# Kernel tuning notes

Hardware: AMD Instinct MI355X
Metric: run time of the kernel (lower is better)

The kernel has to match this reference:

```python
import jax, jax.numpy as jnp
import numpy as np

NUM_V = 20000
N_EDGES = 160000
IN_CH, OUT_CH = 16, 32
IN_ORDER = OUT_ORDER = MID_ORDER = 2
N_RINGS = 2
BAND_LIMIT = 2
NUM_SAMPLES = 7


def build_kernel_basis(n_in, n_out, bl):
    """Equivariant kernel basis [num_bases, 2*bl+1, 2*n_out+1, 2*n_in+1].
    Freq axis layout: [const, cos(t), sin(t), cos(2t), sin(2t), ...] matching precomp."""
    Din, Dout, F = 2 * n_in + 1, 2 * n_out + 1, 2 * bl + 1
    I = np.eye(2)
    E = np.array([[0., -1.], [1., 0.]])   # rotation by pi/2
    S = np.array([[1., 0.], [0., -1.]])   # reflection
    ES = E @ S
    sl = lambda m: slice(0, 1) if m == 0 else slice(2 * m - 1, 2 * m + 1)
    bases = []

    def add(f, cos_blk, sin_blk, m, n):
        if f > bl:
            return
        B = np.zeros((F, Dout, Din))
        if f == 0:
            B[0, sl(m), sl(n)] = cos_blk
        else:
            B[2 * f - 1, sl(m), sl(n)] = cos_blk
            B[2 * f, sl(m), sl(n)] = sin_blk
        bases.append(B)

    for m in range(n_out + 1):
        for n in range(n_in + 1):
            if m == 0 and n == 0:
                add(0, np.ones((1, 1)), None, 0, 0)
            elif n == 0:  # scalar -> order-m pair: R(m t) e1, R(m t) e2
                add(m, np.array([[1.], [0.]]), np.array([[0.], [1.]]), m, 0)
                add(m, np.array([[0.], [1.]]), np.array([[-1.], [0.]]), m, 0)
            elif m == 0:  # order-n pair -> scalar: rows of R(-n t)
                add(n, np.array([[1., 0.]]), np.array([[0., 1.]]), 0, n)
                add(n, np.array([[0., 1.]]), np.array([[-1., 0.]]), 0, n)
            else:
                d = m - n
                f = abs(d)
                sg = 1.0 if d >= 0 else -1.0
                add(f, I, sg * E, m, n)          # R(d t)
                add(f, E, -sg * I, m, n)         # R(d t + pi/2)
                add(m + n, S, ES, m, n)          # R((m+n) t) S
                add(m + n, ES, -S, m, n)         # R((m+n) t + pi/2) S
    return np.stack(bases).astype(np.float32)


def fourier_mats(order, n):
    th = 2 * np.pi * np.arange(n) / n
    cols = [np.ones(n)]
    for m in range(1, order + 1):
        cols += [np.cos(m * th), np.sin(m * th)]
    T = np.stack(cols, 1)                              # [n_samples, 2*order+1]
    scale = np.array([1.0] + [2.0] * (2 * order)) / n
    Tinv = (T * scale).T                               # [2*order+1, n_samples]
    return jnp.asarray(T, jnp.float32), jnp.asarray(Tinv, jnp.float32)


def rep_act(x, alpha, order):
    """Gauge transport: rotate order-m feature pairs by m*alpha. x: [E,C,2*order+1]."""
    parts = [x[:, :, :1]]
    for m in range(1, order + 1):
        c = jnp.cos(m * alpha)[:, None]
        s = jnp.sin(m * alpha)[:, None]
        a, b = x[:, :, 2 * m - 1], x[:, :, 2 * m]
        parts.append(jnp.stack([c * a - s * b, s * a + c * b], axis=-1))
    return jnp.concatenate(parts, axis=-1)


def gem_conv(x, edge_index, precomp, connection, K, W, b, in_order):
    src, dst = edge_index[1], edge_index[0]
    xt = rep_act(x[src], connection, in_order)               # [E, Cin, Din] gather + transport
    wk = jnp.einsum('bfij,broc->froicj', K, W)               # fold basis with ring weights (small)
    t = jnp.einsum('ecj,froicj->efroi', xt, wk)              # per-edge freq/ring responses
    msg = jnp.einsum('efr,efroi->eoi', precomp, t)           # [E, Cout, Dout]
    out = jax.ops.segment_sum(msg, dst, num_segments=NUM_V)  # scatter-add to vertices
    return out.at[:, :, 0].add(b)                            # bias on scalar component


def regular_relu(x, order):
    T, Tinv = fourier_mats(order, NUM_SAMPLES)
    s = jnp.einsum('vcd,sd->vcs', x, T)   # irrep -> regular samples
    return jnp.einsum('vcs,ds->vcd', jax.nn.relu(s), Tinv)


def setup_inputs() -> dict:
    key = jax.random.key(0)
    k = jax.random.split(key, 8)
    nb = build_kernel_basis(IN_ORDER, MID_ORDER, BAND_LIMIT).shape[0]  # 19
    Din = 2 * IN_ORDER + 1
    x = jax.random.normal(k[0], (NUM_V, IN_CH, Din), jnp.float32)
    edge_index = jax.random.randint(k[1], (2, N_EDGES), 0, NUM_V, dtype=jnp.int32)
    precomp = jax.random.normal(k[2], (N_EDGES, 2 * BAND_LIMIT + 1, N_RINGS), jnp.float32)
    connection = jax.random.uniform(k[3], (N_EDGES,), jnp.float32) * (2 * np.pi)
    W1 = jax.random.normal(k[4], (nb, N_RINGS, OUT_CH, IN_CH), jnp.float32) * 0.1
    W2 = jax.random.normal(k[5], (nb, N_RINGS, OUT_CH, OUT_CH), jnp.float32) * 0.05
    W_lin = jax.random.normal(k[6], (OUT_CH, IN_CH), jnp.float32) * 0.1
    zeros = lambda: jnp.zeros((OUT_CH,), jnp.float32)
    return {"x": x, "edge_index": edge_index, "precomp": precomp, "connection": connection,
            "W1": W1, "b1": zeros(), "W2": W2, "b2": zeros(), "W_lin": W_lin, "b_lin": zeros()}


def reference(x, edge_index, precomp, connection, W1, b1, W2, b2, W_lin, b_lin):
    K = jnp.asarray(build_kernel_basis(IN_ORDER, MID_ORDER, BAND_LIMIT))  # orders equal -> shared basis
    y = gem_conv(x, edge_index, precomp, connection, K, W1, b1, IN_ORDER)
    y = regular_relu(y, MID_ORDER)
    y = gem_conv(y, edge_index, precomp, connection, K, W2, b2, MID_ORDER)
    res = jnp.einsum('vcd,oc->vod', x, W_lin) + b_lin[None, :, None]  # 1x1 conv residual
    o = min(y.shape[2], res.shape[2])
    y = y.at[:, :, :o].add(res[:, :, :o])
    return regular_relu(y, OUT_ORDER)
```

## Files before the change

### kernel.cpp

```cpp
#include <hip/hip_runtime.h>
#include <hip/hip_bf16.h>
#include <cstdint>

#define NV     20000
#define NE     160000
#define IC1    16
#define OC     32
#define DIN    5
#define NSLOT  49
#define NOUT   160
struct SlotTables {
    int n;
    int b[64], f[64], i[64], j[64];
    float v[64];
};

constexpr SlotTables make_slots() {
    SlotTables T{};
    float K[19][5][5][5] = {};
    int nb = 0;
    const int BL = 2;
    auto add = [&](int f, const float (*cb)[2], const float (*sb)[2],
                   int m, int n) {
        if (f > BL) return;
        int r0 = (m == 0) ? 0 : (2 * m - 1), nr = (m == 0) ? 1 : 2;
        int c0 = (n == 0) ? 0 : (2 * n - 1), nc = (n == 0) ? 1 : 2;
        for (int a = 0; a < nr; a++)
            for (int bb = 0; bb < nc; bb++) {
                if (f == 0) {
                    K[nb][0][r0 + a][c0 + bb] = cb[a][bb];
                } else {
                    K[nb][2 * f - 1][r0 + a][c0 + bb] = cb[a][bb];
                    K[nb][2 * f    ][r0 + a][c0 + bb] = sb[a][bb];
                }
            }
        nb++;
    };
    const float ONE[2][2]  = {{1, 0}, {0, 0}};
    const float I2[2][2]   = {{1, 0}, {0, 1}};
    const float E2[2][2]   = {{0, -1}, {1, 0}};
    const float S2[2][2]   = {{1, 0}, {0, -1}};
    const float ES2[2][2]  = {{0, 1}, {1, 0}};
    const float NS2[2][2]  = {{-1, 0}, {0, 1}};
    const float C10[2][2]  = {{1, 0}, {0, 0}};
    const float C01[2][2]  = {{0, 0}, {1, 0}};
    const float CM10[2][2] = {{-1, 0}, {0, 0}};
    const float R10[2][2]  = {{1, 0}, {0, 0}};
    const float R01[2][2]  = {{0, 1}, {0, 0}};
    const float RM10[2][2] = {{-1, 0}, {0, 0}};

    for (int m = 0; m <= 2; m++)
        for (int n = 0; n <= 2; n++) {
            if (m == 0 && n == 0) {
                add(0, ONE, ONE, 0, 0);
            } else if (n == 0) {
                add(m, C10, C01, m, 0);
                add(m, C01, CM10, m, 0);
            } else if (m == 0) {
                add(n, R10, R01, 0, n);
                add(n, R01, RM10, 0, n);
            } else {
                int d = m - n;
                int f = d >= 0 ? d : -d;
                float sg = d >= 0 ? 1.f : -1.f;
                const float sgE[2][2]  = {{0, -sg}, {sg, 0}};
                const float msgI[2][2] = {{-sg, 0}, {0, -sg}};
                add(f, I2, sgE, m, n);
                add(f, E2, msgI, m, n);
                add(m + n, S2, ES2, m, n);
                add(m + n, ES2, NS2, m, n);
            }
        }
    T.n = 0;
    for (int i = 0; i < 5; i++)
        for (int b = 0; b < nb; b++)
            for (int f = 0; f < 5; f++)
                for (int j = 0; j < 5; j++)
                    if (K[b][f][i][j] != 0.0f) {
                        T.b[T.n] = b; T.f[T.n] = f; T.i[T.n] = i;
                        T.j[T.n] = j; T.v[T.n] = K[b][f][i][j];
                        T.n++;
                    }
    return T;
}

constexpr SlotTables SL = make_slots();
static_assert(SL.n == NSLOT, "expect 49 kernel-basis nonzeros");

__device__ __forceinline__ uint32_t bf16_rne(float f) {
    uint32_t u = __float_as_uint(f);
    u += 0x7fffu + ((u >> 16) & 1u);
    return u >> 16;
}

typedef __attribute__((ext_vector_type(8))) short bf16x8;
typedef __attribute__((ext_vector_type(4))) float f32x4;

template<int C>
__global__ __launch_bounds__(256) void build_M(const float* __restrict__ W,
                                               float* __restrict__ M) {
    int t = blockIdx.x * 256 + threadIdx.x;
    const int K = C * 50;
    if (t >= K * NOUT) return;
    int n = t % NOUT, k = t / NOUT;
    int o = n / 5, i = n % 5;
    int c = k / 50, r50 = k % 50;
    int j = r50 / 10, q = r50 % 10;
    int f = q >> 1, r = q & 1;
    float acc = 0.f;
    #pragma unroll
    for (int s = 0; s < NSLOT; s++) {
        if (SL.j[s] == j && SL.f[s] == f && SL.i[s] == i)
            acc += SL.v[s] * W[(size_t)((SL.b[s] * 2 + r) * 32 + o) * C + c];
    }
    M[(size_t)k * NOUT + n] = acc;
}

template<int K>
__global__ __launch_bounds__(256) void build_Mfrag(const float* __restrict__ M,
                                                   uint32_t* __restrict__ Mf) {
    int t = blockIdx.x * 256 + threadIdx.x;
    const int total = (K / 32) * 10 * 64 * 4;
    if (t >= total) return;
    int a = t & 3;
    int idx = t >> 2;
    int lane = idx & 63; idx >>= 6;
    int nt = idx % 10;
    int ck = idx / 10;
    int col = nt * 16 + (lane & 15);
    int k0 = ck * 32 + (lane >> 4) * 8 + 2 * a;
    uint32_t lo = bf16_rne(M[(size_t)k0 * NOUT + col]);
    uint32_t hi = bf16_rne(M[(size_t)(k0 + 1) * NOUT + col]);
    Mf[t] = lo | (hi << 16);
}

__global__ __launch_bounds__(256) void hist_k(const int* __restrict__ ei,
                                              int* __restrict__ counts) {
    int e = blockIdx.x * 256 + threadIdx.x;
    if (e < NE) atomicAdd(&counts[ei[e]], 1);
}

__global__ __launch_bounds__(1024) void scan_k(const int* __restrict__ counts,
                                               int* __restrict__ cursor) {
    __shared__ int part[1024];
    int t = threadIdx.x;
    int base = t * 20;
    int local[20];
    int s = 0;
    #pragma unroll
    for (int k = 0; k < 20; k++) {
        int idx = base + k;
        int c = (idx < NV) ? counts[idx] : 0;
        local[k] = c; s += c;
    }
    part[t] = s;
    __syncthreads();
    for (int off = 1; off < 1024; off <<= 1) {
        int add = (t >= off) ? part[t - off] : 0;
        __syncthreads();
        part[t] += add;
        __syncthreads();
    }
    int run = (t == 0) ? 0 : part[t - 1];
    #pragma unroll
    for (int k = 0; k < 20; k++) {
        int idx = base + k;
        if (idx < NV) { cursor[idx] = run; run += local[k]; }
    }
}

__global__ __launch_bounds__(256) void scatter_k(const int* __restrict__ ei,
                                                 int* __restrict__ cursor,
                                                 int* __restrict__ order) {
    int e = blockIdx.x * 256 + threadIdx.x;
    if (e >= NE) return;
    int pos = atomicAdd(&cursor[ei[e]], 1);
    order[pos] = e;
}

__global__ __launch_bounds__(256) void edge_pack(const int* __restrict__ ei,
                                                 const float* __restrict__ pre,
                                                 const float* __restrict__ conn,
                                                 const int* __restrict__ order,
                                                 int* __restrict__ SRC,
                                                 float4* __restrict__ REC) {
    int k = blockIdx.x * 256 + threadIdx.x;
    if (k > NE) return;
    if (k == NE) {
        SRC[NE] = 0;
        REC[(size_t)NE * 3 + 0] = float4{0.f, 0.f, 0.f, 0.f};
        REC[(size_t)NE * 3 + 1] = float4{0.f, 0.f, 0.f, 0.f};
        REC[(size_t)NE * 3 + 2] = float4{0.f, 0.f, 0.f, 0.f};
        return;
    }
    int e = order[k];
    SRC[k] = ei[NE + e];
    float al = conn[e];
    float c1 = __cosf(al), s1 = __sinf(al);
    const float* pp = pre + (size_t)e * 10;
    REC[(size_t)k * 3 + 0] = float4{c1, s1, pp[0], pp[1]};
    REC[(size_t)k * 3 + 1] = float4{pp[2], pp[3], pp[4], pp[5]};
    REC[(size_t)k * 3 + 2] = float4{pp[6], pp[7], pp[8], pp[9]};
}

template<int C>
__global__ __launch_bounds__(256) void zbuild4(const float* __restrict__ xin,
                                               const int*   __restrict__ SRC,
                                               const float4* __restrict__ REC,
                                               const int* __restrict__ cursor,
                                               uint32_t* __restrict__ Z,
                                               int v0, int v1) {
    __shared__ uint32_t st[3200];
    int tid = threadIdx.x;
    int t = blockIdx.x * 256 + tid;
    int pair = t >> 1, h = t & 1;
    int npairs = (v1 - v0) * C;
    bool valid = pair < npairs;
    int c = pair % C;
    int v = v0 + (valid ? pair / C : 0);
    int beg = 0, end = 0;
    if (valid) { beg = (v == 0) ? 0 : cursor[v - 1]; end = cursor[v]; }

    float acc[25];
    #pragma unroll
    for (int z = 0; z < 25; z++) acc[z] = 0.f;

    int k = beg;
    if (k < end) {
        int kn = (k + 1 < end) ? k + 1 : NE;
        int sC = SRC[k];
        int sN = SRC[kn];
        const float4* rp = REC + (size_t)k * 3;
        float4 r0 = rp[0], r1 = rp[1], r2 = rp[2];
        const float* xb = xin + ((size_t)sC * C + c) * DIN;
        float x0 = xb[0], x1 = xb[1], x2 = xb[2], x3 = xb[3], x4 = xb[4];
        while (true) {
            bool more = (k + 1 < end);
            int kn2 = (k + 2 < end) ? k + 2 : NE;
            int sN2 = SRC[kn2];
            const float* xbn = xin + ((size_t)sN * C + c) * DIN;
            float y0 = xbn[0], y1 = xbn[1], y2 = xbn[2], y3 = xbn[3],
                  y4 = xbn[4];
            const float4* rpn = REC + (size_t)kn * 3;
            float4 n0 = rpn[0], n1 = rpn[1], n2 = rpn[2];
            float c1 = r0.x, s1 = r0.y;
            float c2 = c1 * c1 - s1 * s1, s2 = 2.f * c1 * s1;
            float xt[5];
            xt[0] = x0;
            xt[1] = c1 * x1 - s1 * x2;
            xt[2] = s1 * x1 + c1 * x2;
            xt[3] = c2 * x3 - s2 * x4;
            xt[4] = s2 * x3 + c2 * x4;
            float ph[5];
            ph[0] = h ? r1.w : r0.z;
            ph[1] = h ? r2.x : r0.w;
            ph[2] = h ? r2.y : r1.x;
            ph[3] = h ? r2.z : r1.y;
            ph[4] = h ? r2.w : r1.z;
            #pragma unroll
            for (int j = 0; j < 5; j++)
                #pragma unroll
                for (int w = 0; w < 5; w++)
                    acc[j * 5 + w] = fmaf(xt[j], ph[w], acc[j * 5 + w]);
            if (!more) break;
            k += 1;
            r0 = n0; r1 = n1; r2 = n2;
            x0 = y0; x1 = y1; x2 = y2; x3 = y3; x4 = y4;
            sN = sN2; kn = kn2;
        }
    }
    uint32_t* sb = st + (tid >> 1) * 25;
    #pragma unroll
    for (int j = 0; j < 5; j++) {
        float q5v = __shfl_xor(acc[j * 5 + 0], 1);
        if (h == 0) {
            sb[j * 5 + 0] = bf16_rne(acc[j * 5 + 0]) | (bf16_rne(acc[j * 5 + 1]) << 16);
            sb[j * 5 + 1] = bf16_rne(acc[j * 5 + 2]) | (bf16_rne(acc[j * 5 + 3]) << 16);
            sb[j * 5 + 2] = bf16_rne(acc[j * 5 + 4]) | (bf16_rne(q5v) << 16);
        } else {
            sb[j * 5 + 3] = bf16_rne(acc[j * 5 + 1]) | (bf16_rne(acc[j * 5 + 2]) << 16);
            sb[j * 5 + 4] = bf16_rne(acc[j * 5 + 3]) | (bf16_rne(acc[j * 5 + 4]) << 16);
        }
    }
    __syncthreads();
    size_t gbase = (size_t)blockIdx.x * 3200;
    int pbase = blockIdx.x * 128;
    for (int i = tid; i < 3200; i += 256)
        if (pbase + i / 25 < npairs) Z[gbase + i] = st[i];
}

template<int K>
__global__ __launch_bounds__(256) void gemm_mfma(const uint32_t* __restrict__ Z,
                                                 const uint32_t* __restrict__ Mf,
                                                 float* __restrict__ Y,
                                                 int rows) {
    constexpr int NC = K / 32;
    __shared__ uint4 Bs[2][640];
    int t = threadIdx.x;
    int lane = t & 63;
    int wave = t >> 6;
    int r0 = blockIdx.x * 64 + wave * 16;
    int mrow = lane & 15;
    int q = lane >> 4;
    int ra = r0 + mrow;
    if (ra >= rows) ra = rows - 1;
    const uint32_t* za = Z + (size_t)ra * (K / 2) + q * 4;
    const uint4* mfg = (const uint4*)Mf + lane;

    auto stage = [&](int ck, int nb) {
        const uint4* gp = mfg + (size_t)ck * 640;
        for (int i = wave; i < 10; i += 4)
            __builtin_amdgcn_global_load_lds(
                (const __attribute__((address_space(1))) void*)(gp + i * 64),
                (__attribute__((address_space(3))) void*)(&Bs[nb][i * 64]),
                16, 0, 0);
    };

    f32x4 acc[10];
    #pragma unroll
    for (int nt = 0; nt < 10; nt++) acc[nt] = {0.f, 0.f, 0.f, 0.f};

    stage(0, 0);
    bf16x8 af = *(const bf16x8*)za;
    __syncthreads();

    for (int ck = 0; ck < NC; ck++) {
        int buf = ck & 1;
        bf16x8 af_n = af;
        if (ck + 1 < NC) {
            stage(ck + 1, buf ^ 1);
            af_n = *(const bf16x8*)(za + (ck + 1) * 16);
        }
        bf16x8 bf[10];
        #pragma unroll
        for (int nt = 0; nt < 10; nt++)
            bf[nt] = *(const bf16x8*)&Bs[buf][nt * 64 + lane];
        #pragma unroll
        for (int nt = 0; nt < 10; nt++)
            acc[nt] = __builtin_amdgcn_mfma_f32_16x16x32_bf16(af, bf[nt],
                                                              acc[nt], 0, 0, 0);
        af = af_n;
        __syncthreads();
    }
    #pragma unroll
    for (int reg = 0; reg < 4; reg++) {
        int rr = r0 + q * 4 + reg;
        if (rr < rows) {
            float* yb = Y + (size_t)rr * NOUT + (lane & 15);
            #pragma unroll
            for (int nt = 0; nt < 10; nt++) yb[nt * 16] = acc[nt][reg];
        }
    }
}

__device__ __forceinline__ void fourier_relu(float d0, float d1, float d2,
                                             float d3, float d4, float* out5) {
    float o0 = 0, o1 = 0, o2 = 0, o3 = 0, o4 = 0;
    #pragma unroll
    for (int k = 0; k < 7; k++) {
        float th = (float)k * (6.28318530717958647692f / 7.0f);
        float ck = __cosf(th), sk = __sinf(th);
        float c2k = ck * ck - sk * sk, s2k = 2.f * ck * sk;
        float sv = d0 + ck * d1 + sk * d2 + c2k * d3 + s2k * d4;
        sv = fmaxf(sv, 0.f);
        o0 += sv; o1 += sv * ck; o2 += sv * sk; o3 += sv * c2k; o4 += sv * s2k;
    }
    const float i7 = 1.0f / 7.0f;
    out5[0] = o0 * i7; out5[1] = o1 * (2.f * i7); out5[2] = o2 * (2.f * i7);
    out5[3] = o3 * (2.f * i7); out5[4] = o4 * (2.f * i7);
}

__global__ __launch_bounds__(256) void relu_mid(float* __restrict__ y,
                                                const float* __restrict__ b1) {
    int t = blockIdx.x * 256 + threadIdx.x;
    if (t >= NV * 32) return;
    int ch = t & 31;
    float* yb = y + (size_t)t * 5;
    float r[5];
    fourier_relu(yb[0] + b1[ch], yb[1], yb[2], yb[3], yb[4], r);
    #pragma unroll
    for (int d = 0; d < 5; d++) yb[d] = r[d];
}

__global__ __launch_bounds__(256) void final_k(const float* __restrict__ y2,
                                               const float* __restrict__ x,
                                               const float* __restrict__ Wl,
                                               const float* __restrict__ bl,
                                               const float* __restrict__ b2,
                                               float* __restrict__ out) {
    int t = blockIdx.x * 256 + threadIdx.x;
    if (t >= NV * 32) return;
    int o = t & 31;
    int v = t >> 5;
    float r0 = 0, r1 = 0, r2 = 0, r3 = 0, r4 = 0;
    const float* xb = x + (size_t)v * (IC1 * DIN);
    const float* wl = Wl + o * IC1;
    #pragma unroll
    for (int c = 0; c < IC1; c++) {
        float w = wl[c];
        r0 = fmaf(w, xb[c*5+0], r0); r1 = fmaf(w, xb[c*5+1], r1);
        r2 = fmaf(w, xb[c*5+2], r2); r3 = fmaf(w, xb[c*5+3], r3);
        r4 = fmaf(w, xb[c*5+4], r4);
    }
    float blo = bl[o];
    const float* yb = y2 + (size_t)t * 5;
    float d0 = yb[0] + b2[o] + r0 + blo;
    float d1 = yb[1] + r1 + blo;
    float d2 = yb[2] + r2 + blo;
    float d3 = yb[3] + r3 + blo;
    float d4 = yb[4] + r4 + blo;
    float r[5];
    fourier_relu(d0, d1, d2, d3, d4, r);
    float* ob = out + (size_t)t * 5;
    #pragma unroll
    for (int d = 0; d < 5; d++) ob[d] = r[d];
}

extern "C" void kernel_launch(void* const* d_in, const int* in_sizes, int n_in,
                              void* d_out, int out_size, void* d_ws, size_t ws_size,
                              hipStream_t stream) {
    const float* x    = (const float*)d_in[0];
    const int*   ei   = (const int*)  d_in[1];
    const float* pre  = (const float*)d_in[2];
    const float* conn = (const float*)d_in[3];
    const float* W1   = (const float*)d_in[4];
    const float* b1   = (const float*)d_in[5];
    const float* W2   = (const float*)d_in[6];
    const float* b2   = (const float*)d_in[7];
    const float* Wl   = (const float*)d_in[8];
    const float* bl   = (const float*)d_in[9];
    float* out = (float*)d_out;

    const int K1 = IC1 * 50;
    const int K2 = OC  * 50;

    const size_t Y_BYTES   = (size_t)NV * NOUT * sizeof(float);
    const size_t M1_BYTES  = (size_t)K1 * NOUT * sizeof(float);
    const size_t M2_BYTES  = (size_t)K2 * NOUT * sizeof(float);
    const size_t MF1_BYTES = (size_t)(K1 / 32) * 10 * 64 * 16;
    const size_t MF2_BYTES = (size_t)(K2 / 32) * 10 * 64 * 16;
    const size_t CSR_BYTES = (size_t)(2 * NV + NE) * sizeof(int);
    const size_t REC_BYTES = (size_t)(NE + 1) * 48;
    const size_t SRC_BYTES = (((size_t)(NE + 1) * 4 + 15) / 16) * 16;
    char* ws = (char*)d_ws;
    float* y1 = (float*)(ws);
    float* y2 = (float*)(ws + Y_BYTES);
    float* M1 = (float*)(ws + 2 * Y_BYTES);
    float* M2 = (float*)(ws + 2 * Y_BYTES + M1_BYTES);
    uint32_t* Mf1 = (uint32_t*)(ws + 2 * Y_BYTES + M1_BYTES + M2_BYTES);
    uint32_t* Mf2 = (uint32_t*)(ws + 2 * Y_BYTES + M1_BYTES + M2_BYTES + MF1_BYTES);
    int* counts = (int*)(ws + 2 * Y_BYTES + M1_BYTES + M2_BYTES + MF1_BYTES + MF2_BYTES);
    int* cursor = counts + NV;
    int* order  = cursor + NV;
    size_t csr_end = 2 * Y_BYTES + M1_BYTES + M2_BYTES + MF1_BYTES + MF2_BYTES
                   + CSR_BYTES;
    float4* REC = (float4*)(ws + csr_end);
    int*    SRC = (int*)(ws + csr_end + REC_BYTES);
    size_t fixed = csr_end + REC_BYTES + SRC_BYTES;

    size_t tail = (ws_size > fixed) ? (ws_size - fixed) : 0;
    uint32_t* zbuf;
    size_t zcap;
    if (tail >= Y_BYTES) { zbuf = (uint32_t*)(ws + fixed); zcap = tail; }
    else                 { zbuf = (uint32_t*)d_out;        zcap = Y_BYTES; }
    int chunk1 = (int)(zcap / ((size_t)K1 * 2)); if (chunk1 > NV) chunk1 = NV;
    int chunk2 = (int)(zcap / ((size_t)K2 * 2)); if (chunk2 > NV) chunk2 = NV;

    hipMemsetAsync(counts, 0, NV * sizeof(int), stream);

    build_M<IC1><<<(K1 * NOUT + 255) / 256, 256, 0, stream>>>(W1, M1);
    build_M<OC> <<<(K2 * NOUT + 255) / 256, 256, 0, stream>>>(W2, M2);
    build_Mfrag<K1><<<((K1 / 32) * 2560 + 255) / 256, 256, 0, stream>>>(M1, Mf1);
    build_Mfrag<K2><<<((K2 / 32) * 2560 + 255) / 256, 256, 0, stream>>>(M2, Mf2);

    hist_k   <<<(NE + 255) / 256, 256, 0, stream>>>(ei, counts);
    scan_k   <<<1, 1024, 0, stream>>>(counts, cursor);
    scatter_k<<<(NE + 255) / 256, 256, 0, stream>>>(ei, cursor, order);
    edge_pack<<<(NE + 256) / 256, 256, 0, stream>>>(ei, pre, conn, order,
                                                    SRC, REC);

    for (int v0 = 0; v0 < NV; v0 += chunk1) {
        int v1 = v0 + chunk1; if (v1 > NV) v1 = NV;
        int rows = v1 - v0;
        zbuild4<IC1><<<((size_t)rows * IC1 * 2 + 255) / 256, 256, 0, stream>>>(
            x, SRC, REC, cursor, zbuf, v0, v1);
        gemm_mfma<K1><<<(rows + 63) / 64, 256, 0, stream>>>(
            zbuf, Mf1, y1 + (size_t)v0 * NOUT, rows);
    }
    relu_mid<<<(NV * 32 + 255) / 256, 256, 0, stream>>>(y1, b1);
    for (int v0 = 0; v0 < NV; v0 += chunk2) {
        int v1 = v0 + chunk2; if (v1 > NV) v1 = NV;
        int rows = v1 - v0;
        zbuild4<OC><<<((size_t)rows * OC * 2 + 255) / 256, 256, 0, stream>>>(
            y1, SRC, REC, cursor, zbuf, v0, v1);
        gemm_mfma<K2><<<(rows + 63) / 64, 256, 0, stream>>>(
            zbuf, Mf2, y2 + (size_t)v0 * NOUT, rows);
    }
    final_k<<<(NV * 32 + 255) / 256, 256, 0, stream>>>(y2, x, Wl, bl, b2, out);
}
```

Baseline: 282.5 us.

## Fuse edge scatter with packing and gather bf16-packed node features with deeper prefetch

```diff
diff --git a/kernel.cpp b/kernel.cpp
--- a/kernel.cpp
+++ b/kernel.cpp
@@ -169,42 +169,45 @@
     }
 }
 
-__global__ __launch_bounds__(256) void scatter_k(const int* __restrict__ ei,
-                                                 int* __restrict__ cursor,
-                                                 int* __restrict__ order) {
+__global__ __launch_bounds__(256) void scatter_pack(const int* __restrict__ ei,
+                                                    const float* __restrict__ pre,
+                                                    const float* __restrict__ conn,
+                                                    int* __restrict__ cursor,
+                                                    int* __restrict__ SRC,
+                                                    float4* __restrict__ REC) {
     int e = blockIdx.x * 256 + threadIdx.x;
-    if (e >= NE) return;
-    int pos = atomicAdd(&cursor[ei[e]], 1);
-    order[pos] = e;
-}
-
-__global__ __launch_bounds__(256) void edge_pack(const int* __restrict__ ei,
-                                                 const float* __restrict__ pre,
-                                                 const float* __restrict__ conn,
-                                                 const int* __restrict__ order,
-                                                 int* __restrict__ SRC,
-                                                 float4* __restrict__ REC) {
-    int k = blockIdx.x * 256 + threadIdx.x;
-    if (k > NE) return;
-    if (k == NE) {
+    if (e == 0) {
         SRC[NE] = 0;
         REC[(size_t)NE * 3 + 0] = float4{0.f, 0.f, 0.f, 0.f};
         REC[(size_t)NE * 3 + 1] = float4{0.f, 0.f, 0.f, 0.f};
         REC[(size_t)NE * 3 + 2] = float4{0.f, 0.f, 0.f, 0.f};
-        return;
-    }
-    int e = order[k];
-    SRC[k] = ei[NE + e];
+    }
+    if (e >= NE) return;
+    int pos = atomicAdd(&cursor[ei[e]], 1);
+    SRC[pos] = ei[NE + e];
     float al = conn[e];
     float c1 = __cosf(al), s1 = __sinf(al);
     const float* pp = pre + (size_t)e * 10;
-    REC[(size_t)k * 3 + 0] = float4{c1, s1, pp[0], pp[1]};
-    REC[(size_t)k * 3 + 1] = float4{pp[2], pp[3], pp[4], pp[5]};
-    REC[(size_t)k * 3 + 2] = float4{pp[6], pp[7], pp[8], pp[9]};
+    REC[(size_t)pos * 3 + 0] = float4{c1, s1, pp[0], pp[1]};
+    REC[(size_t)pos * 3 + 1] = float4{pp[2], pp[3], pp[4], pp[5]};
+    REC[(size_t)pos * 3 + 2] = float4{pp[6], pp[7], pp[8], pp[9]};
+}
+
+__global__ __launch_bounds__(256) void x_pack(const float* __restrict__ x,
+                                              uint4* __restrict__ xb) {
+    int t = blockIdx.x * 256 + threadIdx.x;
+    if (t >= NV * IC1) return;
+    const float* xr = x + (size_t)t * 5;
+    uint4 o;
+    o.x = bf16_rne(xr[0]) | (bf16_rne(xr[1]) << 16);
+    o.y = bf16_rne(xr[2]) | (bf16_rne(xr[3]) << 16);
+    o.z = bf16_rne(xr[4]);
+    o.w = 0;
+    xb[t] = o;
 }
 
 template<int C>
-__global__ __launch_bounds__(256) void zbuild4(const float* __restrict__ xin,
+__global__ __launch_bounds__(256) void zbuild6(const uint4* __restrict__ xb,
                                                const int*   __restrict__ SRC,
                                                const float4* __restrict__ REC,
                                                const int* __restrict__ cursor,
@@ -227,30 +230,33 @@
 
     int k = beg;
     if (k < end) {
-        int kn = (k + 1 < end) ? k + 1 : NE;
-        int sC = SRC[k];
-        int sN = SRC[kn];
+        int k1 = (k + 1 < end) ? k + 1 : NE;
+        int k2 = (k + 2 < end) ? k + 2 : NE;
+        int s0 = SRC[k], s1i = SRC[k1], s2i = SRC[k2];
         const float4* rp = REC + (size_t)k * 3;
         float4 r0 = rp[0], r1 = rp[1], r2 = rp[2];
-        const float* xb = xin + ((size_t)sC * C + c) * DIN;
-        float x0 = xb[0], x1 = xb[1], x2 = xb[2], x3 = xb[3], x4 = xb[4];
+        uint4 u0 = xb[(size_t)s0 * C + c];
+        uint4 u1 = xb[(size_t)s1i * C + c];
         while (true) {
-            bool more = (k + 1 < end);
-            int kn2 = (k + 2 < end) ? k + 2 : NE;
-            int sN2 = SRC[kn2];
-            const float* xbn = xin + ((size_t)sN * C + c) * DIN;
-            float y0 = xbn[0], y1 = xbn[1], y2 = xbn[2], y3 = xbn[3],
-                  y4 = xbn[4];
-            const float4* rpn = REC + (size_t)kn * 3;
+            bool more = (k1 != NE);
+            int k3 = (k + 3 < end) ? k + 3 : NE;
+            int s3i = SRC[k3];
+            uint4 u2 = xb[(size_t)s2i * C + c];
+            const float4* rpn = REC + (size_t)k1 * 3;
             float4 n0 = rpn[0], n1 = rpn[1], n2 = rpn[2];
-            float c1 = r0.x, s1 = r0.y;
-            float c2 = c1 * c1 - s1 * s1, s2 = 2.f * c1 * s1;
+            float x0 = __uint_as_float(u0.x << 16);
+            float x1 = __uint_as_float(u0.x & 0xffff0000u);
+            float x2 = __uint_as_float(u0.y << 16);
+            float x3 = __uint_as_float(u0.y & 0xffff0000u);
+            float x4 = __uint_as_float(u0.z << 16);
+            float cc1 = r0.x, ss1 = r0.y;
+            float cc2 = cc1 * cc1 - ss1 * ss1, ss2 = 2.f * cc1 * ss1;
             float xt[5];
             xt[0] = x0;
-            xt[1] = c1 * x1 - s1 * x2;
-            xt[2] = s1 * x1 + c1 * x2;
-            xt[3] = c2 * x3 - s2 * x4;
-            xt[4] = s2 * x3 + c2 * x4;
+            xt[1] = cc1 * x1 - ss1 * x2;
+            xt[2] = ss1 * x1 + cc1 * x2;
+            xt[3] = cc2 * x3 - ss2 * x4;
+            xt[4] = ss2 * x3 + cc2 * x4;
             float ph[5];
             ph[0] = h ? r1.w : r0.z;
             ph[1] = h ? r2.x : r0.w;
@@ -263,10 +269,10 @@
                 for (int w = 0; w < 5; w++)
                     acc[j * 5 + w] = fmaf(xt[j], ph[w], acc[j * 5 + w]);
             if (!more) break;
-            k += 1;
+            k = k1; k1 = k2; k2 = k3;
             r0 = n0; r1 = n1; r2 = n2;
-            x0 = y0; x1 = y1; x2 = y2; x3 = y3; x4 = y4;
-            sN = sN2; kn = kn2;
+            u0 = u1; u1 = u2;
+            s2i = s3i;
         }
     }
     uint32_t* sb = st + (tid >> 1) * 25;
@@ -370,16 +376,21 @@
     out5[3] = o3 * (2.f * i7); out5[4] = o4 * (2.f * i7);
 }
 
-__global__ __launch_bounds__(256) void relu_mid(float* __restrict__ y,
-                                                const float* __restrict__ b1) {
+__global__ __launch_bounds__(256) void relu_mid(const float* __restrict__ y,
+                                                const float* __restrict__ b1,
+                                                uint4* __restrict__ yb) {
     int t = blockIdx.x * 256 + threadIdx.x;
     if (t >= NV * 32) return;
     int ch = t & 31;
-    float* yb = y + (size_t)t * 5;
+    const float* yr = y + (size_t)t * 5;
     float r[5];
-    fourier_relu(yb[0] + b1[ch], yb[1], yb[2], yb[3], yb[4], r);
-    #pragma unroll
-    for (int d = 0; d < 5; d++) yb[d] = r[d];
+    fourier_relu(yr[0] + b1[ch], yr[1], yr[2], yr[3], yr[4], r);
+    uint4 o;
+    o.x = bf16_rne(r[0]) | (bf16_rne(r[1]) << 16);
+    o.y = bf16_rne(r[2]) | (bf16_rne(r[3]) << 16);
+    o.z = bf16_rne(r[4]);
+    o.w = 0;
+    yb[t] = o;
 }
 
 __global__ __launch_bounds__(256) void final_k(const float* __restrict__ y2,
@@ -439,24 +450,26 @@
     const size_t M2_BYTES  = (size_t)K2 * NOUT * sizeof(float);
     const size_t MF1_BYTES = (size_t)(K1 / 32) * 10 * 64 * 16;
     const size_t MF2_BYTES = (size_t)(K2 / 32) * 10 * 64 * 16;
-    const size_t CSR_BYTES = (size_t)(2 * NV + NE) * sizeof(int);
+    const size_t CSR_BYTES = (size_t)(2 * NV) * sizeof(int);
     const size_t REC_BYTES = (size_t)(NE + 1) * 48;
     const size_t SRC_BYTES = (((size_t)(NE + 1) * 4 + 15) / 16) * 16;
+    const size_t Y1B_BYTES = (size_t)NV * OC * 16;
     char* ws = (char*)d_ws;
     float* y1 = (float*)(ws);
-    float* y2 = (float*)(ws + Y_BYTES);
-    float* M1 = (float*)(ws + 2 * Y_BYTES);
-    float* M2 = (float*)(ws + 2 * Y_BYTES + M1_BYTES);
-    uint32_t* Mf1 = (uint32_t*)(ws + 2 * Y_BYTES + M1_BYTES + M2_BYTES);
-    uint32_t* Mf2 = (uint32_t*)(ws + 2 * Y_BYTES + M1_BYTES + M2_BYTES + MF1_BYTES);
-    int* counts = (int*)(ws + 2 * Y_BYTES + M1_BYTES + M2_BYTES + MF1_BYTES + MF2_BYTES);
+    float* y2 = y1;
+    float* M1 = (float*)(ws + Y_BYTES);
+    float* M2 = (float*)(ws + Y_BYTES + M1_BYTES);
+    uint32_t* Mf1 = (uint32_t*)(ws + Y_BYTES + M1_BYTES + M2_BYTES);
+    uint32_t* Mf2 = (uint32_t*)(ws + Y_BYTES + M1_BYTES + M2_BYTES + MF1_BYTES);
+    int* counts = (int*)(ws + Y_BYTES + M1_BYTES + M2_BYTES + MF1_BYTES + MF2_BYTES);
     int* cursor = counts + NV;
-    int* order  = cursor + NV;
-    size_t csr_end = 2 * Y_BYTES + M1_BYTES + M2_BYTES + MF1_BYTES + MF2_BYTES
+    size_t csr_end = Y_BYTES + M1_BYTES + M2_BYTES + MF1_BYTES + MF2_BYTES
                    + CSR_BYTES;
     float4* REC = (float4*)(ws + csr_end);
     int*    SRC = (int*)(ws + csr_end + REC_BYTES);
-    size_t fixed = csr_end + REC_BYTES + SRC_BYTES;
+    uint4*  Y1B = (uint4*)(ws + csr_end + REC_BYTES + SRC_BYTES);
+    uint4*  XB1 = Y1B;
+    size_t fixed = csr_end + REC_BYTES + SRC_BYTES + Y1B_BYTES;
 
     size_t tail = (ws_size > fixed) ? (ws_size - fixed) : 0;
     uint32_t* zbuf;
@@ -473,26 +486,26 @@
     build_Mfrag<K1><<<((K1 / 32) * 2560 + 255) / 256, 256, 0, stream>>>(M1, Mf1);
     build_Mfrag<K2><<<((K2 / 32) * 2560 + 255) / 256, 256, 0, stream>>>(M2, Mf2);
 
-    hist_k   <<<(NE + 255) / 256, 256, 0, stream>>>(ei, counts);
-    scan_k   <<<1, 1024, 0, stream>>>(counts, cursor);
-    scatter_k<<<(NE + 255) / 256, 256, 0, stream>>>(ei, cursor, order);
-    edge_pack<<<(NE + 256) / 256, 256, 0, stream>>>(ei, pre, conn, order,
-                                                    SRC, REC);
+    hist_k<<<(NE + 255) / 256, 256, 0, stream>>>(ei, counts);
+    scan_k<<<1, 1024, 0, stream>>>(counts, cursor);
+    scatter_pack<<<(NE + 255) / 256, 256, 0, stream>>>(ei, pre, conn, cursor,
+                                                       SRC, REC);
+    x_pack<<<(NV * IC1 + 255) / 256, 256, 0, stream>>>(x, XB1);
 
     for (int v0 = 0; v0 < NV; v0 += chunk1) {
         int v1 = v0 + chunk1; if (v1 > NV) v1 = NV;
         int rows = v1 - v0;
-        zbuild4<IC1><<<((size_t)rows * IC1 * 2 + 255) / 256, 256, 0, stream>>>(
-            x, SRC, REC, cursor, zbuf, v0, v1);
+        zbuild6<IC1><<<((size_t)rows * IC1 * 2 + 255) / 256, 256, 0, stream>>>(
+            XB1, SRC, REC, cursor, zbuf, v0, v1);
         gemm_mfma<K1><<<(rows + 63) / 64, 256, 0, stream>>>(
             zbuf, Mf1, y1 + (size_t)v0 * NOUT, rows);
     }
-    relu_mid<<<(NV * 32 + 255) / 256, 256, 0, stream>>>(y1, b1);
+    relu_mid<<<(NV * 32 + 255) / 256, 256, 0, stream>>>(y1, b1, Y1B);
     for (int v0 = 0; v0 < NV; v0 += chunk2) {
         int v1 = v0 + chunk2; if (v1 > NV) v1 = NV;
         int rows = v1 - v0;
-        zbuild4<OC><<<((size_t)rows * OC * 2 + 255) / 256, 256, 0, stream>>>(
-            y1, SRC, REC, cursor, zbuf, v0, v1);
+        zbuild6<OC><<<((size_t)rows * OC * 2 + 255) / 256, 256, 0, stream>>>(
+            Y1B, SRC, REC, cursor, zbuf, v0, v1);
         gemm_mfma<K2><<<(rows + 63) / 64, 256, 0, stream>>>(
             zbuf, Mf2, y2 + (size_t)v0 * NOUT, rows);
     }
```

Result: faster. 265.1 us (-6.2%).
